# Optimization experiments

Measured on AMD Instinct MI355X. Metric: run time of the kernel, lower is better.

The kernel has to match this reference:

```python
import jax, jax.numpy as jnp
import numpy as np

B, S, D, H, T, MAXLEN = 8, 1024, 768, 12, 384, 1024
HD = D // H  # spatial head dim = 64
SCALE = HD ** -0.5


def setup_inputs() -> dict:
    key = jax.random.key(0)
    ks = jax.random.split(key, 16)

    def lin(k, din, dout):
        kw, _ = jax.random.split(k)
        w = jax.random.normal(kw, (din, dout), jnp.float32) / np.sqrt(din).astype(np.float32)
        b = jnp.zeros((dout,), jnp.float32)
        return w, b

    Wqs, bqs = lin(ks[0], D, D)
    Wks, bks = lin(ks[1], D, D)
    Wvs, bvs = lin(ks[2], D, D)
    Wqt, bqt = lin(ks[3], T, D)
    Wkt, bkt = lin(ks[4], T, D)
    Wvt, bvt = lin(ks[5], T, D)
    Er = jax.random.normal(ks[6], (MAXLEN, HD), jnp.float32)
    patches = jax.random.normal(ks[7], (B, S, D), jnp.float32)
    time_emb = jax.random.normal(ks[8], (B, T), jnp.float32)
    return dict(patches=patches, time_emb=time_emb,
                Wqs=Wqs, bqs=bqs, Wks=Wks, bks=bks, Wvs=Wvs, bvs=bvs,
                Wqt=Wqt, bqt=bqt, Wkt=Wkt, bkt=bkt, Wvt=Wvt, bvt=bvt, Er=Er)


def _skew(QEr):
    # QEr: [B, H, S, S] -> pad one zero col on the left, reshape, drop first row.
    b, h, r, c = QEr.shape
    padded = jnp.pad(QEr, ((0, 0), (0, 0), (0, 0), (1, 0)))  # [B,H,r,c+1]
    reshaped = padded.reshape(b, h, c + 1, r)
    return reshaped[:, :, 1:, :]  # [B,H,S,S]


def reference(patches, time_emb, Wqs, bqs, Wks, bks, Wvs, bvs,
              Wqt, bqt, Wkt, bkt, Wvt, bvt, Er):
    b, s, _ = patches.shape

    def heads(x):  # [B,S,D] -> [B,H,S,HD]
        return x.reshape(b, -1, H, HD).transpose(0, 2, 1, 3)

    qs = heads(patches @ Wqs + bqs)
    ks = heads(patches @ Wks + bks)
    vs = heads(patches @ Wvs + bvs)
    qt = heads(time_emb @ Wqt + bqt)  # [B,H,1,HD]
    kt = heads(time_emb @ Wkt + bkt)
    vt = heads(time_emb @ Wvt + bvt)

    q = qs + qt
    k = ks + kt
    v = vs + vt

    Er_slice = Er[MAXLEN - s:, :]                      # [S, HD]
    QEr = jnp.einsum('bhsd,td->bhst', qs, Er_slice)    # [B,H,S,S]
    Srel = _skew(QEr)

    scores = (jnp.einsum('bhqd,bhkd->bhqk', q, k) + Srel) * SCALE
    attn = jax.nn.softmax(scores, axis=-1)
    out = jnp.einsum('bhqk,bhkd->bhqd', attn, v)       # [B,H,S,HD]
    return out.transpose(0, 2, 1, 3).reshape(b, s, H * HD)
```

## Files before the change

### kernel.cpp

```cpp
#include <hip/hip_runtime.h>

typedef __attribute__((ext_vector_type(8))) short short8;
typedef __attribute__((ext_vector_type(4))) float floatx4;

#define CSC 0.1803368801f

__device__ __forceinline__ unsigned short f2b(float f){
  unsigned int u = __builtin_bit_cast(unsigned int, f);
  unsigned int r = (u + 0x7fffu + ((u >> 16) & 1u)) >> 16;
  return (unsigned short)r;
}
__device__ __forceinline__ float b2f(unsigned short h){
  unsigned int u = ((unsigned int)h) << 16;
  return __builtin_bit_cast(float, u);
}
__device__ __forceinline__ floatx4 mfma16(short8 a, short8 b, floatx4 c){
  return __builtin_amdgcn_mfma_f32_16x16x32_bf16(a, b, c, 0, 0, 0);
}
__device__ __forceinline__ void gload_lds16(const unsigned short* g, unsigned short* l){
  __builtin_amdgcn_global_load_lds(
      (const __attribute__((address_space(1))) unsigned int*)g,
      (__attribute__((address_space(3))) unsigned int*)l, 16, 0, 0);
}

__global__ __launch_bounds__(256) void transpose_w(
    const float* __restrict__ Wq, const float* __restrict__ Wk,
    const float* __restrict__ Wv, unsigned short* __restrict__ Wb){
  __shared__ float tile[64][65];
  int g = blockIdx.z;
  const float* W = (g==0) ? Wq : (g==1) ? Wk : Wv;
  int r0 = blockIdx.y*64, c0 = blockIdx.x*64;
  int tx = threadIdx.x & 63, ty = threadIdx.x >> 6;
  #pragma unroll
  for (int i=0;i<16;i++){
    int r = i*4 + ty;
    tile[r][tx] = W[(r0+r)*768 + c0 + tx];
  }
  __syncthreads();
  unsigned short* dst = Wb + g*589824;
  #pragma unroll
  for (int i=0;i<16;i++){
    int rr = i*4 + ty;
    dst[(c0+rr)*768 + r0 + tx] = f2b(tile[tx][rr]);
  }
}

__global__ __launch_bounds__(256) void convert_kernel(
    const float* __restrict__ patches, const float* __restrict__ Er,
    const float* __restrict__ temb,
    const float* __restrict__ Wqt, const float* __restrict__ bqt,
    const float* __restrict__ Wkt, const float* __restrict__ bkt,
    const float* __restrict__ Wvt, const float* __restrict__ bvt,
    unsigned short* __restrict__ Pb, unsigned short* __restrict__ Erb,
    float* __restrict__ Tmat){
  int blk = blockIdx.x, tid = threadIdx.x;
  if (blk < 3104){
    const float* src; unsigned short* dst; int idx;
    if (blk < 3072){ idx = blk*2048 + tid*8; src = patches; dst = Pb; }
    else           { idx = (blk-3072)*2048 + tid*8; src = Er; dst = Erb; }
    float4 f0 = *(const float4*)(src + idx);
    float4 f1 = *(const float4*)(src + idx + 4);
    uint4 pk;
    pk.x = (unsigned)f2b(f0.x) | ((unsigned)f2b(f0.y)<<16);
    pk.y = (unsigned)f2b(f0.z) | ((unsigned)f2b(f0.w)<<16);
    pk.z = (unsigned)f2b(f1.x) | ((unsigned)f2b(f1.y)<<16);
    pk.w = (unsigned)f2b(f1.z) | ((unsigned)f2b(f1.w)<<16);
    *(uint4*)(dst + idx) = pk;
  } else {
    int g = (blk-3104)>>3, bb = (blk-3104)&7;
    const float* Wt = (g==0)? Wqt : (g==1)? Wkt : Wvt;
    const float* bt = (g==0)? bqt : (g==1)? bkt : bvt;
    __shared__ float emb[384];
    for (int j=tid;j<384;j+=256) emb[j] = temb[bb*384 + j];
    __syncthreads();
    float acc0 = bt[tid], acc1 = bt[tid+256], acc2 = bt[tid+512];
    for (int t=0;t<384;t++){
      float e = emb[t];
      const float* wr = Wt + t*768;
      acc0 += e*wr[tid]; acc1 += e*wr[tid+256]; acc2 += e*wr[tid+512];
    }
    float* dst = Tmat + g*6144 + bb*768;
    float s = (g==0) ? CSC : 1.0f;
    dst[tid] = acc0*s; dst[tid+256] = acc1*s; dst[tid+512] = acc2*s;
  }
}

__global__ __launch_bounds__(256) void qkv_gemm(
    const unsigned short* __restrict__ Pb, const unsigned short* __restrict__ Wb,
    const float* __restrict__ bq, const float* __restrict__ bk,
    const float* __restrict__ bv, const float* __restrict__ Tmat,
    unsigned short* __restrict__ Qs, unsigned short* __restrict__ K,
    unsigned short* __restrict__ V){
  __shared__ unsigned short smem_q[18432];
  unsigned short* a_lds = smem_q;
  unsigned short* b_lds = smem_q + 8192;
  int g = blockIdx.z;
  int m0 = blockIdx.x*128, n0 = blockIdx.y*128;
  int tid = threadIdx.x, w = tid>>6, lane = tid&63, quad = lane>>4, l16 = lane&15;
  int wr = w>>1, wc = w&1;
  const unsigned short* Wg = Wb + g*589824;
  const float* bias = (g==0)? bq : (g==1)? bk : bv;
  floatx4 acc[4][4];
  #pragma unroll
  for (int i=0;i<4;i++)
    #pragma unroll
    for (int j=0;j<4;j++) acc[i][j] = (floatx4){0.f,0.f,0.f,0.f};

  int rsub = lane>>3, scc = (lane&7)<<3;

  for (int kt=0; kt<12; kt++){
    int k0 = kt*64;
    __syncthreads();
    #pragma unroll
    for (int j=0;j<4;j++){
      int chunk = w*4 + j;
      int r = chunk*8 + rsub;
      gload_lds16(&Pb[(m0+r)*768 + k0 + scc], &a_lds[chunk*512]);
      gload_lds16(&Wg[(n0+r)*768 + k0 + scc], &b_lds[chunk*512]);
    }
    __syncthreads();
    #pragma unroll
    for (int ks=0; ks<2; ks++){
      short8 af[4], bf[4];
      #pragma unroll
      for (int mb=0;mb<4;mb++)
        af[mb] = *(const short8*)&a_lds[(wr*64+mb*16+l16)*64 + ks*32 + quad*8];
      #pragma unroll
      for (int nb=0;nb<4;nb++)
        bf[nb] = *(const short8*)&b_lds[(wc*64+nb*16+l16)*64 + ks*32 + quad*8];
      #pragma unroll
      for (int mb=0;mb<4;mb++)
        #pragma unroll
        for (int nb=0;nb<4;nb++)
          acc[mb][nb] = mfma16(af[mb], bf[nb], acc[mb][nb]);
    }
  }
  if (g < 2){
    #pragma unroll
    for (int mb=0;mb<4;mb++)
    #pragma unroll
    for (int nb=0;nb<4;nb++)
    #pragma unroll
    for (int reg=0;reg<4;reg++){
      int m = m0 + wr*64 + mb*16 + quad*4 + reg;
      int n = n0 + wc*64 + nb*16 + l16;
      int bb = m >> 10, s = m & 1023, h = n >> 6, hd = n & 63;
      float v = acc[mb][nb][reg] + bias[n];
      int base = (bb*12 + h) << 16;
      if (g == 0){
        Qs[base + (s<<6) + hd] = f2b(v * CSC);
      } else {
        float tadd = Tmat[6144 + bb*768 + n];
        K[base + (s<<6) + hd] = f2b(v + tadd);
      }
    }
  } else {
    __syncthreads();
    int bb = m0 >> 10;
    #pragma unroll
    for (int mb=0;mb<4;mb++)
    #pragma unroll
    for (int nb=0;nb<4;nb++)
    #pragma unroll
    for (int reg=0;reg<4;reg++){
      int ml = wr*64 + mb*16 + quad*4 + reg;
      int nl = wc*64 + nb*16 + l16;
      int n = n0 + nl;
      float v = acc[mb][nb][reg] + bias[n] + Tmat[12288 + bb*768 + n];
      smem_q[nl*136 + ml] = f2b(v);
    }
    __syncthreads();
    int s0 = m0 & 1023;
    #pragma unroll
    for (int i=0;i<8;i++){
      int idx = i*256 + tid;
      int r = idx >> 4, c8 = (idx & 15) << 3;
      int n = n0 + r, h = n >> 6, hd = n & 63;
      int base = (bb*12 + h) << 16;
      *(uint4*)&V[base + (hd<<10) + s0 + c8] = *(const uint4*)&smem_q[r*136 + c8];
    }
  }
}

__global__ __launch_bounds__(256, 3) void attn_kernel(
    const unsigned short* __restrict__ Qsp, const unsigned short* __restrict__ Kp,
    const unsigned short* __restrict__ Vtp, const unsigned short* __restrict__ Erb,
    const float* __restrict__ Tq, float* __restrict__ out){
  __shared__ __align__(16) char smem[29696];
  unsigned short* k_lds  = (unsigned short*)smem;
  unsigned short* v_lds  = (unsigned short*)(smem + 9216);
  unsigned short* pw_all = (unsigned short*)(smem + 18432);

  int tid = threadIdx.x, w = tid>>6, lane = tid&63, quad = lane>>4, l16 = lane&15;
  unsigned short* pw = pw_all + w*1408;
  int wg = blockIdx.x;
  int b = wg & 7, slot = wg >> 3;
  int h = slot >> 3, q0 = (slot & 7) << 7;
  int hb = (b*12 + h) << 16;
  const unsigned short* Qsh = Qsp + hb;
  const unsigned short* Kh  = Kp  + hb;
  const unsigned short* Vh  = Vtp + hb;
  const float* tqv = Tq + b*768 + h*64;

  int frow = w*16 + l16;
  short8 qf[2][2], qlo[2][2], qhi[2][2];
  #pragma unroll
  for (int sub=0; sub<2; sub++){
    int qrow = q0 + sub*64 + frow;
    int qrow1 = (qrow < 1023) ? qrow+1 : 1023;
    #pragma unroll
    for (int ks=0; ks<2; ks++){
      int c = ks*32 + quad*8;
      qlo[sub][ks] = *(const short8*)&Qsh[(qrow <<6) + c];
      qhi[sub][ks] = *(const short8*)&Qsh[(qrow1<<6) + c];
      float4 t0 = *(const float4*)&tqv[c];
      float4 t1 = *(const float4*)&tqv[c+4];
      short8 qq;
      qq[0]=(short)f2b(b2f((unsigned short)qlo[sub][ks][0])+t0.x);
      qq[1]=(short)f2b(b2f((unsigned short)qlo[sub][ks][1])+t0.y);
      qq[2]=(short)f2b(b2f((unsigned short)qlo[sub][ks][2])+t0.z);
      qq[3]=(short)f2b(b2f((unsigned short)qlo[sub][ks][3])+t0.w);
      qq[4]=(short)f2b(b2f((unsigned short)qlo[sub][ks][4])+t1.x);
      qq[5]=(short)f2b(b2f((unsigned short)qlo[sub][ks][5])+t1.y);
      qq[6]=(short)f2b(b2f((unsigned short)qlo[sub][ks][6])+t1.z);
      qq[7]=(short)f2b(b2f((unsigned short)qlo[sub][ks][7])+t1.w);
      qf[sub][ks] = qq;
    }
  }

  float lpart[2][4] = {{0.f,0.f,0.f,0.f},{0.f,0.f,0.f,0.f}};
  floatx4 o_acc[2][4];
  #pragma unroll
  for (int sub=0;sub<2;sub++)
    #pragma unroll
    for (int ob=0;ob<4;ob++) o_acc[sub][ob] = (floatx4){0.f,0.f,0.f,0.f};

  int ql = quad*4;
  int ub_lo = 3 - w;

  int sr = tid>>3, scc = (tid&7)<<3;
  uint4 kr0, kr1, vr0, vr1;
  kr0 = *(const uint4*)&Kh[(sr<<6) + scc];
  kr1 = *(const uint4*)&Kh[((sr+32)<<6) + scc];
  vr0 = *(const uint4*)&Vh[(sr<<10) + scc];
  vr1 = *(const uint4*)&Vh[((sr+32)<<10) + scc];

  for (int kt=0; kt<16; kt++){
    int k0 = kt*64;
    __syncthreads();
    *(uint4*)&k_lds[sr*72 + scc]      = kr0;
    *(uint4*)&k_lds[(sr+32)*72 + scc] = kr1;
    *(uint4*)&v_lds[sr*72 + scc]      = vr0;
    *(uint4*)&v_lds[(sr+32)*72 + scc] = vr1;
    __syncthreads();
    int k0n = (kt < 15) ? k0 + 64 : k0;
    kr0 = *(const uint4*)&Kh[((k0n+sr)<<6) + scc];
    kr1 = *(const uint4*)&Kh[((k0n+sr+32)<<6) + scc];
    vr0 = *(const uint4*)&Vh[(sr<<10) + k0n + scc];
    vr1 = *(const uint4*)&Vh[((sr+32)<<10) + k0n + scc];

    floatx4 sc[2][4];
    __builtin_amdgcn_s_setprio(1);
    #pragma unroll
    for (int nb=0;nb<4;nb++){
      sc[0][nb] = (floatx4){0.f,0.f,0.f,0.f};
      sc[1][nb] = (floatx4){0.f,0.f,0.f,0.f};
      #pragma unroll
      for (int ks=0;ks<2;ks++){
        short8 kf = *(const short8*)&k_lds[(nb*16+l16)*72 + ks*32 + quad*8];
        sc[0][nb] = mfma16(qf[0][ks], kf, sc[0][nb]);
        sc[1][nb] = mfma16(qf[1][ks], kf, sc[1][nb]);
      }
    }
    __builtin_amdgcn_s_setprio(0);

    #pragma unroll
    for (int sub=0; sub<2; sub++){
      int diag = k0 - q0 - sub*64;
      bool needL = (diag <= 0), needU = (diag >= 0);
      bool needSel = (diag == 0) || (diag == 64);
      for (int pass=0; pass<2; pass++){
        if ((pass==0 && !needL) || (pass==1 && !needU)) continue;
        int tbase = (pass==0) ? (960 + diag) : (diag - 65);
        const short8* af = (pass==0) ? qlo[sub] : qhi[sub];
        #pragma unroll
        for (int lb=0; lb<5; lb++){
          int ub = ub_lo + lb;
          int t = tbase + ub*16 + l16;
          t = (t < 0) ? 0 : (t > 1023 ? 1023 : t);
          floatx4 pa = (floatx4){0.f,0.f,0.f,0.f};
          #pragma unroll
          for (int ks=0;ks<2;ks++){
            short8 ef = *(const short8*)&Erb[(t<<6) + ks*32 + quad*8];
            pa = mfma16(af[ks], ef, pa);
          }
          #pragma unroll
          for (int reg=0;reg<4;reg++)
            pw[(ql + reg)*88 + lb*16 + l16] = f2b(pa[reg]);
        }
        #pragma unroll
        for (int nb=0;nb<4;nb++)
        #pragma unroll
        for (int reg=0;reg<4;reg++){
          int qlr = ql + reg;
          int ki = nb*16 + l16;
          float bv = b2f(pw[qlr*88 + 15 + ki - qlr]);
          if (needSel){
            int kq = diag + ki - (w*16 + qlr);
            bool sel = (pass==0) ? (kq <= 0) : (kq >= 2);
            bv = sel ? bv : 0.f;
          }
          sc[sub][nb][reg] += bv;
        }
      }
      #pragma unroll
      for (int nb=0;nb<4;nb++)
      #pragma unroll
      for (int reg=0;reg<4;reg++){
        float p = __builtin_amdgcn_exp2f(sc[sub][nb][reg]);
        lpart[sub][reg] += p;
        pw[(ql + reg)*88 + nb*16 + l16] = f2b(p);
      }
      short8 pf[2];
      #pragma unroll
      for (int ks=0;ks<2;ks++)
        pf[ks] = *(const short8*)&pw[l16*88 + ks*32 + quad*8];
      __builtin_amdgcn_s_setprio(1);
      #pragma unroll
      for (int ob=0;ob<4;ob++){
        #pragma unroll
        for (int ks=0;ks<2;ks++){
          short8 vf = *(const short8*)&v_lds[(ob*16+l16)*72 + ks*32 + quad*8];
          o_acc[sub][ob] = mfma16(pf[ks], vf, o_acc[sub][ob]);
        }
      }
      __builtin_amdgcn_s_setprio(0);
    }
  }
  #pragma unroll
  for (int sub=0;sub<2;sub++){
    float rl[4];
    #pragma unroll
    for (int reg=0;reg<4;reg++){
      float l = lpart[sub][reg];
      #pragma unroll
      for (int off=1; off<16; off<<=1) l += __shfl_xor(l, off);
      rl[reg] = __builtin_amdgcn_rcpf(l);
    }
    #pragma unroll
    for (int ob=0;ob<4;ob++)
    #pragma unroll
    for (int reg=0;reg<4;reg++){
      int s = q0 + sub*64 + w*16 + quad*4 + reg;
      out[((b<<10) + s)*768 + (h<<6) + ob*16 + l16] = o_acc[sub][ob][reg] * rl[reg];
    }
  }
}

extern "C" void kernel_launch(void* const* d_in, const int* in_sizes, int n_in,
                              void* d_out, int out_size, void* d_ws, size_t ws_size,
                              hipStream_t stream) {
  const float* patches  = (const float*)d_in[0];
  const float* time_emb = (const float*)d_in[1];
  const float* Wqs = (const float*)d_in[2];  const float* bqs = (const float*)d_in[3];
  const float* Wks = (const float*)d_in[4];  const float* bks = (const float*)d_in[5];
  const float* Wvs = (const float*)d_in[6];  const float* bvs = (const float*)d_in[7];
  const float* Wqt = (const float*)d_in[8];  const float* bqt = (const float*)d_in[9];
  const float* Wkt = (const float*)d_in[10]; const float* bkt = (const float*)d_in[11];
  const float* Wvt = (const float*)d_in[12]; const float* bvt = (const float*)d_in[13];
  const float* Er  = (const float*)d_in[14];

  unsigned short* Qsp  = (unsigned short*)d_ws;
  unsigned short* Kp   = Qsp + 6291456;
  unsigned short* Vp   = Kp  + 6291456;
  unsigned short* Wbp  = Vp  + 6291456;
  unsigned short* Erbp = Wbp + 1769472;
  unsigned short* Pbp  = Erbp + 65536;
  float*          Tmat = (float*)(Pbp + 6291456);

  float* out = (float*)d_out;

  hipLaunchKernelGGL(convert_kernel, dim3(3128), dim3(256), 0, stream,
                     patches, Er, time_emb, Wqt, bqt, Wkt, bkt, Wvt, bvt,
                     Pbp, Erbp, Tmat);
  hipLaunchKernelGGL(transpose_w, dim3(12,12,3), dim3(256), 0, stream,
                     Wqs, Wks, Wvs, Wbp);
  hipLaunchKernelGGL(qkv_gemm, dim3(64,6,3), dim3(256), 0, stream,
                     Pbp, Wbp, bqs, bks, bvs, Tmat, Qsp, Kp, Vp);
  hipLaunchKernelGGL(attn_kernel, dim3(768), dim3(256), 0, stream,
                     Qsp, Kp, Vp, Erbp, Tmat, out);
}
```

Measured before the change: 334.9 us.

## Halve attention query tile to double grid, and XOR-swizzle GEMM LDS tiles

The attention kernel now processes 64 query rows per workgroup instead of 128. That doubles the grid to 1536 blocks, cuts register use, and raises the launch-bounds occupancy hint from 3 to 5. Separately, the QKV GEMM XOR-swizzles its LDS column chunks on both the global-to-LDS load and the fragment reads to avoid bank conflicts. The cost is that each K/V tile is loaded into LDS twice as often per query row, since each block now reuses it for fewer rows.

```diff
diff --git a/kernel.cpp b/kernel.cpp
--- a/kernel.cpp
+++ b/kernel.cpp
@@ -106,7 +106,9 @@
     #pragma unroll
     for (int j=0;j<4;j++) acc[i][j] = (floatx4){0.f,0.f,0.f,0.f};
 
-  int rsub = lane>>3, scc = (lane&7)<<3;
+  int rsub = lane>>3;
+  int csw  = (((lane&7) ^ rsub) << 3);
+  int sw   = l16 & 7;
 
   for (int kt=0; kt<12; kt++){
     int k0 = kt*64;
@@ -115,19 +117,20 @@
     for (int j=0;j<4;j++){
       int chunk = w*4 + j;
       int r = chunk*8 + rsub;
-      gload_lds16(&Pb[(m0+r)*768 + k0 + scc], &a_lds[chunk*512]);
-      gload_lds16(&Wg[(n0+r)*768 + k0 + scc], &b_lds[chunk*512]);
+      gload_lds16(&Pb[(m0+r)*768 + k0 + csw], &a_lds[chunk*512]);
+      gload_lds16(&Wg[(n0+r)*768 + k0 + csw], &b_lds[chunk*512]);
     }
     __syncthreads();
     #pragma unroll
     for (int ks=0; ks<2; ks++){
       short8 af[4], bf[4];
+      int cc = ((ks*4 + quad) ^ sw) << 3;
       #pragma unroll
       for (int mb=0;mb<4;mb++)
-        af[mb] = *(const short8*)&a_lds[(wr*64+mb*16+l16)*64 + ks*32 + quad*8];
+        af[mb] = *(const short8*)&a_lds[(wr*64+mb*16+l16)*64 + cc];
       #pragma unroll
       for (int nb=0;nb<4;nb++)
-        bf[nb] = *(const short8*)&b_lds[(wc*64+nb*16+l16)*64 + ks*32 + quad*8];
+        bf[nb] = *(const short8*)&b_lds[(wc*64+nb*16+l16)*64 + cc];
       #pragma unroll
       for (int mb=0;mb<4;mb++)
         #pragma unroll
@@ -182,7 +185,7 @@
   }
 }
 
-__global__ __launch_bounds__(256, 3) void attn_kernel(
+__global__ __launch_bounds__(256, 5) void attn_kernel(
     const unsigned short* __restrict__ Qsp, const unsigned short* __restrict__ Kp,
     const unsigned short* __restrict__ Vtp, const unsigned short* __restrict__ Erb,
     const float* __restrict__ Tq, float* __restrict__ out){
@@ -195,7 +198,7 @@
   unsigned short* pw = pw_all + w*1408;
   int wg = blockIdx.x;
   int b = wg & 7, slot = wg >> 3;
-  int h = slot >> 3, q0 = (slot & 7) << 7;
+  int h = slot >> 4, q0 = (slot & 15) << 6;
   int hb = (b*12 + h) << 16;
   const unsigned short* Qsh = Qsp + hb;
   const unsigned short* Kh  = Kp  + hb;
@@ -203,37 +206,34 @@
   const float* tqv = Tq + b*768 + h*64;
 
   int frow = w*16 + l16;
-  short8 qf[2][2], qlo[2][2], qhi[2][2];
-  #pragma unroll
-  for (int sub=0; sub<2; sub++){
-    int qrow = q0 + sub*64 + frow;
+  short8 qf[2], qlo[2], qhi[2];
+  {
+    int qrow = q0 + frow;
     int qrow1 = (qrow < 1023) ? qrow+1 : 1023;
     #pragma unroll
     for (int ks=0; ks<2; ks++){
       int c = ks*32 + quad*8;
-      qlo[sub][ks] = *(const short8*)&Qsh[(qrow <<6) + c];
-      qhi[sub][ks] = *(const short8*)&Qsh[(qrow1<<6) + c];
+      qlo[ks] = *(const short8*)&Qsh[(qrow <<6) + c];
+      qhi[ks] = *(const short8*)&Qsh[(qrow1<<6) + c];
       float4 t0 = *(const float4*)&tqv[c];
       float4 t1 = *(const float4*)&tqv[c+4];
       short8 qq;
-      qq[0]=(short)f2b(b2f((unsigned short)qlo[sub][ks][0])+t0.x);
-      qq[1]=(short)f2b(b2f((unsigned short)qlo[sub][ks][1])+t0.y);
-      qq[2]=(short)f2b(b2f((unsigned short)qlo[sub][ks][2])+t0.z);
-      qq[3]=(short)f2b(b2f((unsigned short)qlo[sub][ks][3])+t0.w);
-      qq[4]=(short)f2b(b2f((unsigned short)qlo[sub][ks][4])+t1.x);
-      qq[5]=(short)f2b(b2f((unsigned short)qlo[sub][ks][5])+t1.y);
-      qq[6]=(short)f2b(b2f((unsigned short)qlo[sub][ks][6])+t1.z);
-      qq[7]=(short)f2b(b2f((unsigned short)qlo[sub][ks][7])+t1.w);
-      qf[sub][ks] = qq;
-    }
-  }
-
-  float lpart[2][4] = {{0.f,0.f,0.f,0.f},{0.f,0.f,0.f,0.f}};
-  floatx4 o_acc[2][4];
+      qq[0]=(short)f2b(b2f((unsigned short)qlo[ks][0])+t0.x);
+      qq[1]=(short)f2b(b2f((unsigned short)qlo[ks][1])+t0.y);
+      qq[2]=(short)f2b(b2f((unsigned short)qlo[ks][2])+t0.z);
+      qq[3]=(short)f2b(b2f((unsigned short)qlo[ks][3])+t0.w);
+      qq[4]=(short)f2b(b2f((unsigned short)qlo[ks][4])+t1.x);
+      qq[5]=(short)f2b(b2f((unsigned short)qlo[ks][5])+t1.y);
+      qq[6]=(short)f2b(b2f((unsigned short)qlo[ks][6])+t1.z);
+      qq[7]=(short)f2b(b2f((unsigned short)qlo[ks][7])+t1.w);
+      qf[ks] = qq;
+    }
+  }
+
+  float lpart[4] = {0.f,0.f,0.f,0.f};
+  floatx4 o_acc[4];
   #pragma unroll
-  for (int sub=0;sub<2;sub++)
-    #pragma unroll
-    for (int ob=0;ob<4;ob++) o_acc[sub][ob] = (floatx4){0.f,0.f,0.f,0.f};
+  for (int ob=0;ob<4;ob++) o_acc[ob] = (floatx4){0.f,0.f,0.f,0.f};
 
   int ql = quad*4;
   int ub_lo = 3 - w;
@@ -259,90 +259,84 @@
     vr0 = *(const uint4*)&Vh[(sr<<10) + k0n + scc];
     vr1 = *(const uint4*)&Vh[((sr+32)<<10) + k0n + scc];
 
-    floatx4 sc[2][4];
+    floatx4 sc[4];
     __builtin_amdgcn_s_setprio(1);
     #pragma unroll
     for (int nb=0;nb<4;nb++){
-      sc[0][nb] = (floatx4){0.f,0.f,0.f,0.f};
-      sc[1][nb] = (floatx4){0.f,0.f,0.f,0.f};
+      sc[nb] = (floatx4){0.f,0.f,0.f,0.f};
       #pragma unroll
       for (int ks=0;ks<2;ks++){
         short8 kf = *(const short8*)&k_lds[(nb*16+l16)*72 + ks*32 + quad*8];
-        sc[0][nb] = mfma16(qf[0][ks], kf, sc[0][nb]);
-        sc[1][nb] = mfma16(qf[1][ks], kf, sc[1][nb]);
+        sc[nb] = mfma16(qf[ks], kf, sc[nb]);
       }
     }
     __builtin_amdgcn_s_setprio(0);
 
-    #pragma unroll
-    for (int sub=0; sub<2; sub++){
-      int diag = k0 - q0 - sub*64;
-      bool needL = (diag <= 0), needU = (diag >= 0);
-      bool needSel = (diag == 0) || (diag == 64);
-      for (int pass=0; pass<2; pass++){
-        if ((pass==0 && !needL) || (pass==1 && !needU)) continue;
-        int tbase = (pass==0) ? (960 + diag) : (diag - 65);
-        const short8* af = (pass==0) ? qlo[sub] : qhi[sub];
+    int diag = k0 - q0;
+    bool needL = (diag <= 0), needU = (diag >= 0);
+    bool needSel = (diag == 0) || (diag == 64);
+    for (int pass=0; pass<2; pass++){
+      if ((pass==0 && !needL) || (pass==1 && !needU)) continue;
+      int tbase = (pass==0) ? (960 + diag) : (diag - 65);
+      const short8* af = (pass==0) ? qlo : qhi;
+      #pragma unroll
+      for (int lb=0; lb<5; lb++){
+        int ub = ub_lo + lb;
+        int t = tbase + ub*16 + l16;
+        t = (t < 0) ? 0 : (t > 1023 ? 1023 : t);
+        floatx4 pa = (floatx4){0.f,0.f,0.f,0.f};
         #pragma unroll
-        for (int lb=0; lb<5; lb++){
-          int ub = ub_lo + lb;
-          int t = tbase + ub*16 + l16;
-          t = (t < 0) ? 0 : (t > 1023 ? 1023 : t);
-          floatx4 pa = (floatx4){0.f,0.f,0.f,0.f};
-          #pragma unroll
-          for (int ks=0;ks<2;ks++){
-            short8 ef = *(const short8*)&Erb[(t<<6) + ks*32 + quad*8];
-            pa = mfma16(af[ks], ef, pa);
-          }
-          #pragma unroll
-          for (int reg=0;reg<4;reg++)
-            pw[(ql + reg)*88 + lb*16 + l16] = f2b(pa[reg]);
+        for (int ks=0;ks<2;ks++){
+          short8 ef = *(const short8*)&Erb[(t<<6) + ks*32 + quad*8];
+          pa = mfma16(af[ks], ef, pa);
         }
         #pragma unroll
-        for (int nb=0;nb<4;nb++)
-        #pragma unroll
-        for (int reg=0;reg<4;reg++){
-          int qlr = ql + reg;
-          int ki = nb*16 + l16;
-          float bv = b2f(pw[qlr*88 + 15 + ki - qlr]);
-          if (needSel){
-            int kq = diag + ki - (w*16 + qlr);
-            bool sel = (pass==0) ? (kq <= 0) : (kq >= 2);
-            bv = sel ? bv : 0.f;
-          }
-          sc[sub][nb][reg] += bv;
+        for (int reg=0;reg<4;reg++)
+          pw[(ql + reg)*88 + lb*16 + l16] = f2b(pa[reg]);
+      }
+      #pragma unroll
+      for (int nb=0;nb<4;nb++)
+      #pragma unroll
+      for (int reg=0;reg<4;reg++){
+        int qlr = ql + reg;
+        int ki = nb*16 + l16;
+        float bv = b2f(pw[qlr*88 + 15 + ki - qlr]);
+        if (needSel){
+          int kq = diag + ki - (w*16 + qlr);
+          bool sel = (pass==0) ? (kq <= 0) : (kq >= 2);
+          bv = sel ? bv : 0.f;
         }
-      }
-      #pragma unroll
-      for (int nb=0;nb<4;nb++)
-      #pragma unroll
-      for (int reg=0;reg<4;reg++){
-        float p = __builtin_amdgcn_exp2f(sc[sub][nb][reg]);
-        lpart[sub][reg] += p;
-        pw[(ql + reg)*88 + nb*16 + l16] = f2b(p);
-      }
-      short8 pf[2];
-      #pragma unroll
-      for (int ks=0;ks<2;ks++)
-        pf[ks] = *(const short8*)&pw[l16*88 + ks*32 + quad*8];
-      __builtin_amdgcn_s_setprio(1);
-      #pragma unroll
-      for (int ob=0;ob<4;ob++){
-        #pragma unroll
-        for (int ks=0;ks<2;ks++){
-          short8 vf = *(const short8*)&v_lds[(ob*16+l16)*72 + ks*32 + quad*8];
-          o_acc[sub][ob] = mfma16(pf[ks], vf, o_acc[sub][ob]);
-        }
-      }
-      __builtin_amdgcn_s_setprio(0);
-    }
-  }
-  #pragma unroll
-  for (int sub=0;sub<2;sub++){
+        sc[nb][reg] += bv;
+      }
+    }
+    #pragma unroll
+    for (int nb=0;nb<4;nb++)
+    #pragma unroll
+    for (int reg=0;reg<4;reg++){
+      float p = __builtin_amdgcn_exp2f(sc[nb][reg]);
+      lpart[reg] += p;
+      pw[(ql + reg)*88 + nb*16 + l16] = f2b(p);
+    }
+    short8 pf[2];
+    #pragma unroll
+    for (int ks=0;ks<2;ks++)
+      pf[ks] = *(const short8*)&pw[l16*88 + ks*32 + quad*8];
+    __builtin_amdgcn_s_setprio(1);
+    #pragma unroll
+    for (int ob=0;ob<4;ob++){
+      #pragma unroll
+      for (int ks=0;ks<2;ks++){
+        short8 vf = *(const short8*)&v_lds[(ob*16+l16)*72 + ks*32 + quad*8];
+        o_acc[ob] = mfma16(pf[ks], vf, o_acc[ob]);
+      }
+    }
+    __builtin_amdgcn_s_setprio(0);
+  }
+  {
     float rl[4];
     #pragma unroll
     for (int reg=0;reg<4;reg++){
-      float l = lpart[sub][reg];
+      float l = lpart[reg];
       #pragma unroll
       for (int off=1; off<16; off<<=1) l += __shfl_xor(l, off);
       rl[reg] = __builtin_amdgcn_rcpf(l);
@@ -351,8 +345,8 @@
     for (int ob=0;ob<4;ob++)
     #pragma unroll
     for (int reg=0;reg<4;reg++){
-      int s = q0 + sub*64 + w*16 + quad*4 + reg;
-      out[((b<<10) + s)*768 + (h<<6) + ob*16 + l16] = o_acc[sub][ob][reg] * rl[reg];
+      int s = q0 + w*16 + quad*4 + reg;
+      out[((b<<10) + s)*768 + (h<<6) + ob*16 + l16] = o_acc[ob][reg] * rl[reg];
     }
   }
 }
@@ -387,6 +381,6 @@
                      Wqs, Wks, Wvs, Wbp);
   hipLaunchKernelGGL(qkv_gemm, dim3(64,6,3), dim3(256), 0, stream,
                      Pbp, Wbp, bqs, bks, bvs, Tmat, Qsp, Kp, Vp);
-  hipLaunchKernelGGL(attn_kernel, dim3(768), dim3(256), 0, stream,
+  hipLaunchKernelGGL(attn_kernel, dim3(1536), dim3(256), 0, stream,
                      Qsp, Kp, Vp, Erbp, Tmat, out);
 }
```

Measured after the change: 415.2 us. +24.0%, slower.

## Double-buffer K/V tiles in attention and XOR-swizzle QKV GEMM LDS

Applied to the files above, without the earlier changes.

The attention kernel now keeps two K/V LDS buffers. The next tile is written to LDS and the tile after that is prefetched from global memory while MFMAs run on the current buffer, which cuts one of the two barriers per iteration. The projection GEMM also XOR-swizzles the column chunks it writes to LDS through global_load_lds and reads back, to avoid LDS bank conflicts. LDS use in the attention kernel grows to about 47KB, which may lower occupancy under launch_bounds(256,3).

```diff
diff --git a/kernel.cpp b/kernel.cpp
--- a/kernel.cpp
+++ b/kernel.cpp
@@ -106,7 +106,9 @@
     #pragma unroll
     for (int j=0;j<4;j++) acc[i][j] = (floatx4){0.f,0.f,0.f,0.f};
 
-  int rsub = lane>>3, scc = (lane&7)<<3;
+  int rsub = lane>>3;
+  int csw  = (((lane&7) ^ rsub) << 3);
+  int sw   = l16 & 7;
 
   for (int kt=0; kt<12; kt++){
     int k0 = kt*64;
@@ -115,19 +117,20 @@
     for (int j=0;j<4;j++){
       int chunk = w*4 + j;
       int r = chunk*8 + rsub;
-      gload_lds16(&Pb[(m0+r)*768 + k0 + scc], &a_lds[chunk*512]);
-      gload_lds16(&Wg[(n0+r)*768 + k0 + scc], &b_lds[chunk*512]);
+      gload_lds16(&Pb[(m0+r)*768 + k0 + csw], &a_lds[chunk*512]);
+      gload_lds16(&Wg[(n0+r)*768 + k0 + csw], &b_lds[chunk*512]);
     }
     __syncthreads();
     #pragma unroll
     for (int ks=0; ks<2; ks++){
       short8 af[4], bf[4];
+      int cc = ((ks*4 + quad) ^ sw) << 3;
       #pragma unroll
       for (int mb=0;mb<4;mb++)
-        af[mb] = *(const short8*)&a_lds[(wr*64+mb*16+l16)*64 + ks*32 + quad*8];
+        af[mb] = *(const short8*)&a_lds[(wr*64+mb*16+l16)*64 + cc];
       #pragma unroll
       for (int nb=0;nb<4;nb++)
-        bf[nb] = *(const short8*)&b_lds[(wc*64+nb*16+l16)*64 + ks*32 + quad*8];
+        bf[nb] = *(const short8*)&b_lds[(wc*64+nb*16+l16)*64 + cc];
       #pragma unroll
       for (int mb=0;mb<4;mb++)
         #pragma unroll
@@ -186,10 +189,8 @@
     const unsigned short* __restrict__ Qsp, const unsigned short* __restrict__ Kp,
     const unsigned short* __restrict__ Vtp, const unsigned short* __restrict__ Erb,
     const float* __restrict__ Tq, float* __restrict__ out){
-  __shared__ __align__(16) char smem[29696];
-  unsigned short* k_lds  = (unsigned short*)smem;
-  unsigned short* v_lds  = (unsigned short*)(smem + 9216);
-  unsigned short* pw_all = (unsigned short*)(smem + 18432);
+  __shared__ __align__(16) char smem[48128];
+  unsigned short* pw_all = (unsigned short*)(smem + 36864);
 
   int tid = threadIdx.x, w = tid>>6, lane = tid&63, quad = lane>>4, l16 = lane&15;
   unsigned short* pw = pw_all + w*1408;
@@ -244,20 +245,40 @@
   kr1 = *(const uint4*)&Kh[((sr+32)<<6) + scc];
   vr0 = *(const uint4*)&Vh[(sr<<10) + scc];
   vr1 = *(const uint4*)&Vh[((sr+32)<<10) + scc];
+  {
+    unsigned short* k0p = (unsigned short*)smem;
+    unsigned short* v0p = (unsigned short*)(smem + 9216);
+    *(uint4*)&k0p[sr*72 + scc]      = kr0;
+    *(uint4*)&k0p[(sr+32)*72 + scc] = kr1;
+    *(uint4*)&v0p[sr*72 + scc]      = vr0;
+    *(uint4*)&v0p[(sr+32)*72 + scc] = vr1;
+  }
+  kr0 = *(const uint4*)&Kh[((64+sr)<<6) + scc];
+  kr1 = *(const uint4*)&Kh[((64+sr+32)<<6) + scc];
+  vr0 = *(const uint4*)&Vh[(sr<<10) + 64 + scc];
+  vr1 = *(const uint4*)&Vh[((sr+32)<<10) + 64 + scc];
+  __syncthreads();
 
   for (int kt=0; kt<16; kt++){
     int k0 = kt*64;
-    __syncthreads();
-    *(uint4*)&k_lds[sr*72 + scc]      = kr0;
-    *(uint4*)&k_lds[(sr+32)*72 + scc] = kr1;
-    *(uint4*)&v_lds[sr*72 + scc]      = vr0;
-    *(uint4*)&v_lds[(sr+32)*72 + scc] = vr1;
-    __syncthreads();
-    int k0n = (kt < 15) ? k0 + 64 : k0;
-    kr0 = *(const uint4*)&Kh[((k0n+sr)<<6) + scc];
-    kr1 = *(const uint4*)&Kh[((k0n+sr+32)<<6) + scc];
-    vr0 = *(const uint4*)&Vh[(sr<<10) + k0n + scc];
-    vr1 = *(const uint4*)&Vh[((sr+32)<<10) + k0n + scc];
+    int cur = kt & 1;
+    unsigned short* k_lds = (unsigned short*)(smem + cur*18432);
+    unsigned short* v_lds = (unsigned short*)(smem + cur*18432 + 9216);
+    if (kt < 15){
+      unsigned short* kn = (unsigned short*)(smem + (cur^1)*18432);
+      unsigned short* vn = (unsigned short*)(smem + (cur^1)*18432 + 9216);
+      *(uint4*)&kn[sr*72 + scc]      = kr0;
+      *(uint4*)&kn[(sr+32)*72 + scc] = kr1;
+      *(uint4*)&vn[sr*72 + scc]      = vr0;
+      *(uint4*)&vn[(sr+32)*72 + scc] = vr1;
+      if (kt < 14){
+        int t2 = k0 + 128;
+        kr0 = *(const uint4*)&Kh[((t2+sr)<<6) + scc];
+        kr1 = *(const uint4*)&Kh[((t2+sr+32)<<6) + scc];
+        vr0 = *(const uint4*)&Vh[(sr<<10) + t2 + scc];
+        vr1 = *(const uint4*)&Vh[((sr+32)<<10) + t2 + scc];
+      }
+    }
 
     floatx4 sc[2][4];
     __builtin_amdgcn_s_setprio(1);
@@ -336,6 +357,7 @@
       }
       __builtin_amdgcn_s_setprio(0);
     }
+    if (kt < 15) __syncthreads();
   }
   #pragma unroll
   for (int sub=0;sub<2;sub++){
```

Result: slower. 349.2 us (+4.3%).

## Double-buffer QKV GEMM with swizzled LDS and fuse weight transpose into prep

Applied to the files above, without the earlier changes.

The QKV GEMM now uses two LDS buffers, prefetching the next K-tile with global_load_lds while the current one is computed, and applies an XOR swizzle to the column layout to reduce LDS bank conflicts. The separate weight-transpose kernel is folded into the conversion kernel as extra blocks, which saves one launch. A small unroll pragma is added to the time-embedding loop. LDS use per block roughly doubles, which may lower occupancy.

```diff
diff --git a/kernel.cpp b/kernel.cpp
--- a/kernel.cpp
+++ b/kernel.cpp
@@ -23,36 +23,16 @@
       (__attribute__((address_space(3))) unsigned int*)l, 16, 0, 0);
 }
 
-__global__ __launch_bounds__(256) void transpose_w(
-    const float* __restrict__ Wq, const float* __restrict__ Wk,
-    const float* __restrict__ Wv, unsigned short* __restrict__ Wb){
-  __shared__ float tile[64][65];
-  int g = blockIdx.z;
-  const float* W = (g==0) ? Wq : (g==1) ? Wk : Wv;
-  int r0 = blockIdx.y*64, c0 = blockIdx.x*64;
-  int tx = threadIdx.x & 63, ty = threadIdx.x >> 6;
-  #pragma unroll
-  for (int i=0;i<16;i++){
-    int r = i*4 + ty;
-    tile[r][tx] = W[(r0+r)*768 + c0 + tx];
-  }
-  __syncthreads();
-  unsigned short* dst = Wb + g*589824;
-  #pragma unroll
-  for (int i=0;i<16;i++){
-    int rr = i*4 + ty;
-    dst[(c0+rr)*768 + r0 + tx] = f2b(tile[tx][rr]);
-  }
-}
-
-__global__ __launch_bounds__(256) void convert_kernel(
+__global__ __launch_bounds__(256) void prep_kernel(
     const float* __restrict__ patches, const float* __restrict__ Er,
     const float* __restrict__ temb,
     const float* __restrict__ Wqt, const float* __restrict__ bqt,
     const float* __restrict__ Wkt, const float* __restrict__ bkt,
     const float* __restrict__ Wvt, const float* __restrict__ bvt,
+    const float* __restrict__ Wqs, const float* __restrict__ Wks,
+    const float* __restrict__ Wvs,
     unsigned short* __restrict__ Pb, unsigned short* __restrict__ Erb,
-    float* __restrict__ Tmat){
+    float* __restrict__ Tmat, unsigned short* __restrict__ Wb){
   int blk = blockIdx.x, tid = threadIdx.x;
   if (blk < 3104){
     const float* src; unsigned short* dst; int idx;
@@ -66,7 +46,7 @@
     pk.z = (unsigned)f2b(f1.x) | ((unsigned)f2b(f1.y)<<16);
     pk.w = (unsigned)f2b(f1.z) | ((unsigned)f2b(f1.w)<<16);
     *(uint4*)(dst + idx) = pk;
-  } else {
+  } else if (blk < 3128){
     int g = (blk-3104)>>3, bb = (blk-3104)&7;
     const float* Wt = (g==0)? Wqt : (g==1)? Wkt : Wvt;
     const float* bt = (g==0)? bqt : (g==1)? bkt : bvt;
@@ -74,6 +54,7 @@
     for (int j=tid;j<384;j+=256) emb[j] = temb[bb*384 + j];
     __syncthreads();
     float acc0 = bt[tid], acc1 = bt[tid+256], acc2 = bt[tid+512];
+    #pragma unroll 4
     for (int t=0;t<384;t++){
       float e = emb[t];
       const float* wr = Wt + t*768;
@@ -82,6 +63,26 @@
     float* dst = Tmat + g*6144 + bb*768;
     float s = (g==0) ? CSC : 1.0f;
     dst[tid] = acc0*s; dst[tid+256] = acc1*s; dst[tid+512] = acc2*s;
+  } else {
+    int tb = blk - 3128;
+    int g = tb / 144, rem = tb % 144;
+    int by = rem / 12, bx = rem % 12;
+    __shared__ float tile[64][65];
+    const float* W = (g==0) ? Wqs : (g==1) ? Wks : Wvs;
+    int r0 = by*64, c0 = bx*64;
+    int tx = tid & 63, ty = tid >> 6;
+    #pragma unroll
+    for (int i=0;i<16;i++){
+      int r = i*4 + ty;
+      tile[r][tx] = W[(r0+r)*768 + c0 + tx];
+    }
+    __syncthreads();
+    unsigned short* dst = Wb + g*589824;
+    #pragma unroll
+    for (int i=0;i<16;i++){
+      int rr = i*4 + ty;
+      dst[(c0+rr)*768 + r0 + tx] = f2b(tile[tx][rr]);
+    }
   }
 }
 
@@ -91,9 +92,7 @@
     const float* __restrict__ bv, const float* __restrict__ Tmat,
     unsigned short* __restrict__ Qs, unsigned short* __restrict__ K,
     unsigned short* __restrict__ V){
-  __shared__ unsigned short smem_q[18432];
-  unsigned short* a_lds = smem_q;
-  unsigned short* b_lds = smem_q + 8192;
+  __shared__ unsigned short smem_q[32768];
   int g = blockIdx.z;
   int m0 = blockIdx.x*128, n0 = blockIdx.y*128;
   int tid = threadIdx.x, w = tid>>6, lane = tid&63, quad = lane>>4, l16 = lane&15;
@@ -106,34 +105,53 @@
     #pragma unroll
     for (int j=0;j<4;j++) acc[i][j] = (floatx4){0.f,0.f,0.f,0.f};
 
-  int rsub = lane>>3, scc = (lane&7)<<3;
-
+  int rsub = lane>>3;
+  int csw  = (((lane&7) ^ rsub) << 3);
+  int sw   = l16 & 7;
+
+  #pragma unroll
+  for (int j=0;j<4;j++){
+    int chunk = w*4 + j;
+    int r = chunk*8 + rsub;
+    gload_lds16(&Pb[(m0+r)*768 + csw],        &smem_q[chunk*512]);
+    gload_lds16(&Wg[(n0+r)*768 + csw],        &smem_q[8192 + chunk*512]);
+  }
+  __syncthreads();
+
+  int cur = 0;
   for (int kt=0; kt<12; kt++){
-    int k0 = kt*64;
-    __syncthreads();
-    #pragma unroll
-    for (int j=0;j<4;j++){
-      int chunk = w*4 + j;
-      int r = chunk*8 + rsub;
-      gload_lds16(&Pb[(m0+r)*768 + k0 + scc], &a_lds[chunk*512]);
-      gload_lds16(&Wg[(n0+r)*768 + k0 + scc], &b_lds[chunk*512]);
-    }
-    __syncthreads();
+    if (kt < 11){
+      int k0n = (kt+1)*64;
+      unsigned short* an = smem_q + (cur^1)*16384;
+      unsigned short* bn = an + 8192;
+      #pragma unroll
+      for (int j=0;j<4;j++){
+        int chunk = w*4 + j;
+        int r = chunk*8 + rsub;
+        gload_lds16(&Pb[(m0+r)*768 + k0n + csw], &an[chunk*512]);
+        gload_lds16(&Wg[(n0+r)*768 + k0n + csw], &bn[chunk*512]);
+      }
+    }
+    const unsigned short* a_lds = smem_q + cur*16384;
+    const unsigned short* b_lds = a_lds + 8192;
     #pragma unroll
     for (int ks=0; ks<2; ks++){
       short8 af[4], bf[4];
+      int cc = ((ks*4 + quad) ^ sw) << 3;
       #pragma unroll
       for (int mb=0;mb<4;mb++)
-        af[mb] = *(const short8*)&a_lds[(wr*64+mb*16+l16)*64 + ks*32 + quad*8];
+        af[mb] = *(const short8*)&a_lds[(wr*64+mb*16+l16)*64 + cc];
       #pragma unroll
       for (int nb=0;nb<4;nb++)
-        bf[nb] = *(const short8*)&b_lds[(wc*64+nb*16+l16)*64 + ks*32 + quad*8];
+        bf[nb] = *(const short8*)&b_lds[(wc*64+nb*16+l16)*64 + cc];
       #pragma unroll
       for (int mb=0;mb<4;mb++)
         #pragma unroll
         for (int nb=0;nb<4;nb++)
           acc[mb][nb] = mfma16(af[mb], bf[nb], acc[mb][nb]);
     }
+    __syncthreads();
+    cur ^= 1;
   }
   if (g < 2){
     #pragma unroll
@@ -155,7 +173,6 @@
       }
     }
   } else {
-    __syncthreads();
     int bb = m0 >> 10;
     #pragma unroll
     for (int mb=0;mb<4;mb++)
@@ -380,11 +397,9 @@
 
   float* out = (float*)d_out;
 
-  hipLaunchKernelGGL(convert_kernel, dim3(3128), dim3(256), 0, stream,
+  hipLaunchKernelGGL(prep_kernel, dim3(3560), dim3(256), 0, stream,
                      patches, Er, time_emb, Wqt, bqt, Wkt, bkt, Wvt, bvt,
-                     Pbp, Erbp, Tmat);
-  hipLaunchKernelGGL(transpose_w, dim3(12,12,3), dim3(256), 0, stream,
-                     Wqs, Wks, Wvs, Wbp);
+                     Wqs, Wks, Wvs, Pbp, Erbp, Tmat, Wbp);
   hipLaunchKernelGGL(qkv_gemm, dim3(64,6,3), dim3(256), 0, stream,
                      Pbp, Wbp, bqs, bks, bvs, Tmat, Qsp, Kp, Vp);
   hipLaunchKernelGGL(attn_kernel, dim3(768), dim3(256), 0, stream,
```

New measurement: 324.6 us. 1.03x faster.
